# Kernel tuning notes

Hardware: AMD Instinct MI355X
Metric: run time of the kernel (lower is better)

Reference implementation:

```python
import jax, jax.numpy as jnp
import numpy as np

SEQ_LEN, BATCH, VOCAB = 128, 32, 32000
EMB, HID = 32, 16


def setup_inputs() -> dict:
    key = jax.random.key(0)
    ks = jax.random.split(key, 10)
    return {
        "input_batch": jax.random.randint(ks[0], (SEQ_LEN, BATCH), 0, VOCAB, dtype=jnp.int64)
        if jax.config.jax_enable_x64 else jax.random.randint(ks[0], (SEQ_LEN, BATCH), 0, VOCAB, dtype=jnp.int32),
        "h0_lr": jax.random.uniform(ks[1], (BATCH, HID), dtype=jnp.float32),
        "h0_rl": jax.random.uniform(ks[2], (BATCH, HID), dtype=jnp.float32),
        "embedding": jax.random.normal(ks[3], (VOCAB, EMB), dtype=jnp.float32),
        "W_lr": jax.random.normal(ks[4], (HID, EMB + HID), dtype=jnp.float32) * 0.25,
        "b_lr": jax.random.normal(ks[5], (HID,), dtype=jnp.float32) * 0.25,
        "W_rl": jax.random.normal(ks[6], (HID, EMB + HID), dtype=jnp.float32) * 0.25,
        "b_rl": jax.random.normal(ks[7], (HID,), dtype=jnp.float32) * 0.25,
        "W_ho": jax.random.normal(ks[8], (VOCAB, 2 * HID), dtype=jnp.float32) * 0.25,
        "b_ho": jax.random.normal(ks[9], (VOCAB,), dtype=jnp.float32) * 0.25,
    }


def _rnn_step(W, b):
    # h_{t+1} = tanh([x_t, h_t] @ W^T + b)
    def f(h, x):
        h_new = jnp.tanh(jnp.concatenate([x, h], axis=-1) @ W.T + b)
        return h_new, h_new
    return f


def reference(input_batch, h0_lr, h0_rl, embedding, W_lr, b_lr, W_rl, b_rl, W_ho, b_ho):
    emb = embedding[input_batch]  # [S, B, EMB]
    # Left-to-right: consumes emb[0..S-2]; hLR[0] = h0_lr, len S
    _, hs_lr = jax.lax.scan(_rnn_step(W_lr, b_lr), h0_lr, emb[:-1])
    hLR = jnp.concatenate([h0_lr[None], hs_lr], axis=0)  # [S, B, HID]
    # Right-to-left: consumes emb[S-1 .. 1]; hRL[0] = h0_rl, len S
    _, hs_rl = jax.lax.scan(_rnn_step(W_rl, b_rl), h0_rl, emb[:0:-1])
    hRL = jnp.concatenate([h0_rl[None], hs_rl], axis=0)  # [S, B, HID]
    # prediction[i] pairs hLR[i] with hRL[S-1-i]
    combined = jnp.concatenate([hLR, hRL[::-1]], axis=-1)  # [S, B, 2*HID]
    logits = combined @ W_ho.T + b_ho  # [S, B, VOCAB]
    return jax.nn.log_softmax(logits, axis=-1)
```

## Files before the change

kernel.cpp:

```cpp
#include <hip/hip_runtime.h>
#include <hip/hip_bf16.h>
#include <math.h>

#define SS 128
#define BB 32
#define VV 32000
#define EE 32
#define HH 16
#define KK 32
#define NROWS (SS*BB)
#define NSL 16
#define VT 125
#define NPRE 8

typedef __attribute__((ext_vector_type(4))) float f32x4;
typedef __attribute__((ext_vector_type(8))) short bf16x8;
typedef __attribute__((ext_vector_type(4))) short s16x4;

#define DPPF(x, ctrl) __builtin_bit_cast(float, __builtin_amdgcn_update_dpp( \
    __builtin_bit_cast(int, (x)), __builtin_bit_cast(int, (x)), (ctrl), 0xF, 0xF, false))

__global__ __launch_bounds__(256) void k_prep(
    const float* __restrict__ Who, __hip_bfloat16* __restrict__ who_bf,
    const int* __restrict__ tok, const float* __restrict__ emb,
    const float* __restrict__ Wlr, const float* __restrict__ blr,
    const float* __restrict__ Wrl, const float* __restrict__ brl,
    float* __restrict__ xp) {
  if (blockIdx.x < 1000) {
    int i = blockIdx.x * 256 + threadIdx.x;
    f32x4 v = ((const f32x4*)Who)[i];
    s16x4 o;
    #pragma unroll
    for (int q = 0; q < 4; ++q) {
      __hip_bfloat16 h = __float2bfloat16(v[q]);
      o[q] = *reinterpret_cast<short*>(&h);
    }
    ((s16x4*)who_bf)[i] = o;
  } else {
    int g = (blockIdx.x - 1000) * 256 + threadIdx.x;
    int dir = g >> 16;
    int rem = g & 65535;
    int t = rem >> 9;
    int b = (rem >> 4) & 31;
    int j = rem & 15;
    const float* W  = dir ? Wrl : Wlr;
    const float* bv = dir ? brl : blr;
    int tk = tok[t*BB + b];
    const float* er = emb + tk*EE;
    const float* wr = W + j*(EE+HH);
    float acc = bv[j];
    #pragma unroll
    for (int k = 0; k < EE; ++k) acc += er[k] * wr[k];
    xp[g] = acc;
  }
}

__global__ __launch_bounds__(128) void k_rnn_fused(
    const float* __restrict__ xp,
    const float* __restrict__ h0lr, const float* __restrict__ h0rl,
    const float* __restrict__ Wlr, const float* __restrict__ Wrl,
    __hip_bfloat16* __restrict__ comb_bf) {
  int bid = blockIdx.x;
  int dir = bid >> 2;
  int b = (bid & 3) * 8 + (threadIdx.x >> 4);
  int j = threadIdx.x & 15;
  const float* W  = dir ? Wrl : Wlr;
  const float* h0 = dir ? h0rl : h0lr;
  float wr[HH];
  #pragma unroll
  for (int r = 0; r < HH; ++r) wr[r] = W[j*(EE+HH) + EE + (j ^ r)];
  const float* x = xp + dir * (SS*BB*HH);
  int u = b*HH + j;
  float h = h0[u];
  if (dir == 0) comb_bf[0*(BB*KK) + b*KK + j] = __float2bfloat16(h);
  else          comb_bf[(SS-1)*(BB*KK) + b*KK + HH + j] = __float2bfloat16(h);
  float xbuf[NPRE];
  #pragma unroll
  for (int p = 0; p < NPRE; ++p) {
    int tt = 1 + p;
    int off = dir ? (SS-tt)*(BB*HH) + u : (tt-1)*(BB*HH) + u;
    xbuf[p] = x[off];
  }
  for (int tc = 1; tc < SS; tc += NPRE) {
    #pragma unroll
    for (int i = 0; i < NPRE; ++i) {
      int t = tc + i;
      if (t < SS) {
        float xv = xbuf[i];
        int tp = t + NPRE;
        int offp = (tp < SS) ? (dir ? (SS-tp)*(BB*HH) + u : (tp-1)*(BB*HH) + u) : u;
        xbuf[i] = x[offp];
        float t1  = DPPF(h, 0xB1);
        float t2  = DPPF(h, 0x4E);
        float t3  = DPPF(h, 0x1B);
        float t7  = DPPF(h, 0x141);
        float t15 = DPPF(h, 0x140);
        float t4  = DPPF(t7, 0x1B);
        float t5  = DPPF(t7, 0x4E);
        float t6  = DPPF(t7, 0xB1);
        float t8  = DPPF(t15, 0x141);
        float t12 = DPPF(t15, 0x1B);
        float t13 = DPPF(t15, 0x4E);
        float t14 = DPPF(t15, 0xB1);
        float t9  = DPPF(t8, 0xB1);
        float t10 = DPPF(t8, 0x4E);
        float t11 = DPPF(t8, 0x1B);
        float a0 = fmaf(wr[0], h,  xv);
        a0 = fmaf(wr[4],  t4,  a0);
        a0 = fmaf(wr[8],  t8,  a0);
        a0 = fmaf(wr[12], t12, a0);
        float a1 = wr[1] * t1;
        a1 = fmaf(wr[5],  t5,  a1);
        a1 = fmaf(wr[9],  t9,  a1);
        a1 = fmaf(wr[13], t13, a1);
        float a2 = wr[2] * t2;
        a2 = fmaf(wr[6],  t6,  a2);
        a2 = fmaf(wr[10], t10, a2);
        a2 = fmaf(wr[14], t14, a2);
        float a3 = wr[3] * t3;
        a3 = fmaf(wr[7],  t7,  a3);
        a3 = fmaf(wr[11], t11, a3);
        a3 = fmaf(wr[15], t15, a3);
        float acc = (a0 + a1) + (a2 + a3);
        float e = __expf(2.f * acc);
        h = fmaf(-2.f, __builtin_amdgcn_rcpf(e + 1.f), 1.f);
        int ci = dir ? ((SS-1-t)*(BB*KK) + b*KK + HH + j)
                     : (t*(BB*KK) + b*KK + j);
        comb_bf[ci] = __float2bfloat16(h);
      }
    }
  }
}

__global__ __launch_bounds__(256) void k_sumexp(
    const __hip_bfloat16* __restrict__ cb, const __hip_bfloat16* __restrict__ wb,
    const float* __restrict__ bho, float* __restrict__ part) {
  int wg = ((blockIdx.x & 7) << 7) | (blockIdx.x >> 3);
  int w = wg * 4 + (threadIdx.x >> 6);
  int lane = threadIdx.x & 63;
  int rt = w >> 4;
  int sl = w & 15;
  int v0 = sl * (VT*16);
  int g = lane >> 4, c = lane & 15;
  bf16x8 bfr = *(const bf16x8*)(cb + (size_t)(rt*16 + c)*KK + g*8);
  float s = 0.f;
  for (int t = 0; t < VT; ++t) {
    int v = v0 + t*16;
    bf16x8 af = *(const bf16x8*)(wb + (size_t)(v + c)*KK + g*8);
    f32x4 bh = *(const f32x4*)(bho + v + g*4);
    f32x4 d = __builtin_amdgcn_mfma_f32_16x16x32_bf16(af, bfr, bh, 0, 0, 0);
    s += __expf(d[0]) + __expf(d[1]) + __expf(d[2]) + __expf(d[3]);
  }
  s += __shfl_xor(s, 16);
  s += __shfl_xor(s, 32);
  if (lane < 16)
    part[(size_t)(rt*16 + lane)*NSL + sl] = s;
}

__global__ __launch_bounds__(256) void k_write(
    const __hip_bfloat16* __restrict__ cb, const __hip_bfloat16* __restrict__ wb,
    const float* __restrict__ bho, const float* __restrict__ part,
    float* __restrict__ out) {
  int wg = ((blockIdx.x & 7) << 7) | (blockIdx.x >> 3);
  int w = wg * 4 + (threadIdx.x >> 6);
  int lane = threadIdx.x & 63;
  int rt = w >> 4;
  int sl = w & 15;
  int v0 = sl * (VT*16);
  int g = lane >> 4, c = lane & 15;
  size_t row = rt*16 + c;
  const f32x4* pp = (const f32x4*)(part + row*NSL);
  f32x4 p0 = pp[0], p1 = pp[1], p2 = pp[2], p3 = pp[3];
  float s = (p0[0]+p0[1]+p0[2]+p0[3]) + (p1[0]+p1[1]+p1[2]+p1[3])
          + (p2[0]+p2[1]+p2[2]+p2[3]) + (p3[0]+p3[1]+p3[2]+p3[3]);
  float Lr = logf(s);
  bf16x8 bfr = *(const bf16x8*)(cb + row*KK + g*8);
  for (int t = 0; t < VT; ++t) {
    int v = v0 + t*16;
    bf16x8 af = *(const bf16x8*)(wb + (size_t)(v + c)*KK + g*8);
    f32x4 bh = *(const f32x4*)(bho + v + g*4);
    f32x4 cin = bh - Lr;
    f32x4 d = __builtin_amdgcn_mfma_f32_16x16x32_bf16(af, bfr, cin, 0, 0, 0);
    *(f32x4*)(out + row*VV + v + g*4) = d;
  }
}

extern "C" void kernel_launch(void* const* d_in, const int* in_sizes, int n_in,
                              void* d_out, int out_size, void* d_ws, size_t ws_size,
                              hipStream_t stream) {
  const int*   tok  = (const int*)d_in[0];
  const float* h0lr = (const float*)d_in[1];
  const float* h0rl = (const float*)d_in[2];
  const float* emb  = (const float*)d_in[3];
  const float* Wlr  = (const float*)d_in[4];
  const float* blr  = (const float*)d_in[5];
  const float* Wrl  = (const float*)d_in[6];
  const float* brl  = (const float*)d_in[7];
  const float* Who  = (const float*)d_in[8];
  const float* bho  = (const float*)d_in[9];
  float* out = (float*)d_out;
  float* ws  = (float*)d_ws;

  float* xp   = ws;
  float* part = ws + 131072;
  __hip_bfloat16* comb_bf = (__hip_bfloat16*)(ws + 196608);
  __hip_bfloat16* who_bf  = (__hip_bfloat16*)(ws + 262144);

  hipLaunchKernelGGL(k_prep, dim3(1512), dim3(256), 0, stream,
                     Who, who_bf, tok, emb, Wlr, blr, Wrl, brl, xp);
  hipLaunchKernelGGL(k_rnn_fused, dim3(8), dim3(128), 0, stream,
                     xp, h0lr, h0rl, Wlr, Wrl, comb_bf);
  hipLaunchKernelGGL(k_sumexp, dim3(1024), dim3(256), 0, stream,
                     comb_bf, who_bf, bho, part);
  hipLaunchKernelGGL(k_write, dim3(1024), dim3(256), 0, stream,
                     comb_bf, who_bf, bho, part, out);
}
```

Measured before the change: 214.2 us.

## Stage W_ho slices in swizzled LDS per block in write kernel

The write kernel now gives each block a 50-tile vocabulary slice. The block loads that slice of bf16 W_ho and bias into LDS once, using an XOR-swizzled layout, and its four waves reuse it across four row tiles. The grid grows from 1024 to 2560 blocks. The aim is to cut redundant global/L2 reads of W_ho and keep the output-store stream busy, at the cost of about 50KB of LDS per block, which limits occupancy, plus a sync and staging overhead.

Result: faster. 192.6 us (-10.1%).

```diff
diff --git a/kernel.cpp b/kernel.cpp
--- a/kernel.cpp
+++ b/kernel.cpp
@@ -12,6 +12,8 @@
 #define NSL 16
 #define VT 125
 #define NPRE 8
+#define WSL 40
+#define WVT 50
 
 typedef __attribute__((ext_vector_type(4))) float f32x4;
 typedef __attribute__((ext_vector_type(8))) short bf16x8;
@@ -161,27 +163,43 @@
     const __hip_bfloat16* __restrict__ cb, const __hip_bfloat16* __restrict__ wb,
     const float* __restrict__ bho, const float* __restrict__ part,
     float* __restrict__ out) {
-  int wg = ((blockIdx.x & 7) << 7) | (blockIdx.x >> 3);
-  int w = wg * 4 + (threadIdx.x >> 6);
-  int lane = threadIdx.x & 63;
-  int rt = w >> 4;
-  int sl = w & 15;
-  int v0 = sl * (VT*16);
+  __shared__ char afl[WVT * 1024];
+  __shared__ float bhl[WVT * 16];
+  int bid = blockIdx.x;
+  int wg = ((bid & 7) * 320) + (bid >> 3);
+  int rtg = wg / WSL;
+  int sl  = wg % WSL;
+  int v0  = sl * (WVT*16);
+  int tid = threadIdx.x;
+  const f32x4* src = (const f32x4*)(wb + (size_t)v0 * KK);
+  for (int o = tid; o < WVT*64; o += 256) {
+    f32x4 v = src[o];
+    int t = o >> 6, u = o & 63;
+    int us = u ^ ((u >> 3) & 7);
+    *(f32x4*)(afl + t*1024 + us*16) = v;
+  }
+  for (int o = tid; o < WVT*16; o += 256) bhl[o] = bho[v0 + o];
+  __syncthreads();
+  int wid = tid >> 6, lane = tid & 63;
+  int rt = rtg*4 + wid;
   int g = lane >> 4, c = lane & 15;
-  size_t row = rt*16 + c;
+  size_t row = (size_t)rt*16 + c;
   const f32x4* pp = (const f32x4*)(part + row*NSL);
   f32x4 p0 = pp[0], p1 = pp[1], p2 = pp[2], p3 = pp[3];
   float s = (p0[0]+p0[1]+p0[2]+p0[3]) + (p1[0]+p1[1]+p1[2]+p1[3])
           + (p2[0]+p2[1]+p2[2]+p2[3]) + (p3[0]+p3[1]+p3[2]+p3[3]);
   float Lr = logf(s);
   bf16x8 bfr = *(const bf16x8*)(cb + row*KK + g*8);
-  for (int t = 0; t < VT; ++t) {
-    int v = v0 + t*16;
-    bf16x8 af = *(const bf16x8*)(wb + (size_t)(v + c)*KK + g*8);
-    f32x4 bh = *(const f32x4*)(bho + v + g*4);
+  int u = c*4 + g;
+  int us = u ^ ((u >> 3) & 7);
+  const char* afp = afl + us*16;
+  float* op = out + row*VV + v0 + g*4;
+  for (int t = 0; t < WVT; ++t) {
+    bf16x8 a = *(const bf16x8*)(afp + t*1024);
+    f32x4 bh = *(const f32x4*)(bhl + t*16 + g*4);
     f32x4 cin = bh - Lr;
-    f32x4 d = __builtin_amdgcn_mfma_f32_16x16x32_bf16(af, bfr, cin, 0, 0, 0);
-    *(f32x4*)(out + row*VV + v + g*4) = d;
+    f32x4 d = __builtin_amdgcn_mfma_f32_16x16x32_bf16(a, bfr, cin, 0, 0, 0);
+    *(f32x4*)(op + t*16) = d;
   }
 }
 
@@ -212,6 +230,6 @@
                      xp, h0lr, h0rl, Wlr, Wrl, comb_bf);
   hipLaunchKernelGGL(k_sumexp, dim3(1024), dim3(256), 0, stream,
                      comb_bf, who_bf, bho, part);
-  hipLaunchKernelGGL(k_write, dim3(1024), dim3(256), 0, stream,
+  hipLaunchKernelGGL(k_write, dim3(2560), dim3(256), 0, stream,
                      comb_bf, who_bf, bho, part, out);
 }
```
